# Kernel optimization log

Measured on AMD Instinct MI355X. Metric: run time of the kernel, lower is better.

Reference implementation:

```python
import jax, jax.numpy as jnp
from jax import lax
import numpy as np

B, M = 16384, 200            # flattened batch (B*TT), tokens per observation
NUM_LAYERS, GW, GH = 22, 11, 11
CNN_CH, HIDDEN = 128, 512
ACTION_NVEC = (9, 10)

MAX_VEC = jnp.array([9.0, 1.0, 1.0, 10.0, 3.0, 254.0, 1.0, 1.0, 235.0, 8.0, 9.0,
                     250.0, 29.0, 1.0, 1.0, 8.0, 1.0, 1.0, 6.0, 3.0, 1.0, 2.0],
                    jnp.float32)[None, :, None, None]  # [1,22,1,1]


def setup_inputs() -> dict:
    key = jax.random.key(0)
    ks = jax.random.split(key, 16)
    # compose coords byte so x,y nibbles are valid grid indices (0..10)
    xs = jax.random.randint(ks[0], (B, M), 0, GW)
    ys = jax.random.randint(ks[1], (B, M), 0, GH)
    coords = xs * 16 + ys
    atr = jax.random.randint(ks[2], (B, M), 0, NUM_LAYERS)
    val = jax.random.randint(ks[3], (B, M), 0, 11)
    observations = jnp.stack([coords, atr, val], axis=-1).astype(jnp.int32)  # [B,M,3]

    def nrm(k, shape, std=0.02):
        return (jax.random.normal(k, shape, jnp.float32) * std)

    return {
        "observations": observations,
        "conv1_w": nrm(ks[4], (CNN_CH, NUM_LAYERS, 5, 5)),
        "conv1_b": jnp.zeros((CNN_CH,), jnp.float32),
        "conv2_w": nrm(ks[5], (CNN_CH, CNN_CH, 3, 3)),
        "conv2_b": jnp.zeros((CNN_CH,), jnp.float32),
        "fc_w": nrm(ks[6], (HIDDEN // 2, CNN_CH)),
        "fc_b": jnp.zeros((HIDDEN // 2,), jnp.float32),
        "self_w": nrm(ks[7], (HIDDEN // 2, NUM_LAYERS)),
        "self_b": jnp.zeros((HIDDEN // 2,), jnp.float32),
        "actor0_w": nrm(ks[8], (ACTION_NVEC[0], HIDDEN), std=0.01),
        "actor0_b": jnp.zeros((ACTION_NVEC[0],), jnp.float32),
        "actor1_w": nrm(ks[9], (ACTION_NVEC[1], HIDDEN), std=0.01),
        "actor1_b": jnp.zeros((ACTION_NVEC[1],), jnp.float32),
        "value_w": nrm(ks[10], (1, HIDDEN)),
        "value_b": jnp.zeros((1,), jnp.float32),
    }


def reference(observations, conv1_w, conv1_b, conv2_w, conv2_b, fc_w, fc_b,
              self_w, self_b, actor0_w, actor0_b, actor1_w, actor1_b,
              value_w, value_b):
    obs = jnp.where(observations == 255, 0, observations)
    coords = obs[..., 0]
    xs = (coords >> 4) & 15
    ys = coords & 15
    atr = obs[..., 1]
    vals = obs[..., 2].astype(jnp.float32)           # [B,M]
    Bt = obs.shape[0]
    b_idx = jnp.broadcast_to(jnp.arange(Bt)[:, None], vals.shape)
    # masked scatter into dense grid (all tokens valid after 255->0 clamp)
    box = jnp.zeros((Bt, NUM_LAYERS, GW, GH), jnp.float32)
    box = box.at[b_idx, atr, xs, ys].set(vals, mode="drop")
    feats = box / MAX_VEC                            # [B,22,11,11]

    self_f = jax.nn.relu(feats[:, :, 5, 5] @ self_w.T + self_b)  # [B,256]

    dn = ("NCHW", "OIHW", "NCHW")
    h = lax.conv_general_dilated(feats, conv1_w, (3, 3), "VALID", dimension_numbers=dn)
    h = jax.nn.relu(h + conv1_b[None, :, None, None])            # [B,128,3,3]
    h = lax.conv_general_dilated(h, conv2_w, (1, 1), "VALID", dimension_numbers=dn)
    h = jax.nn.relu(h + conv2_b[None, :, None, None])            # [B,128,1,1]
    h = h.reshape(Bt, -1)
    cnn_f = jax.nn.relu(h @ fc_w.T + fc_b)                       # [B,256]

    hidden = jnp.concatenate([self_f, cnn_f], axis=1)            # [B,512]
    logits0 = hidden @ actor0_w.T + actor0_b
    logits1 = hidden @ actor1_w.T + actor1_b
    value = hidden @ value_w.T + value_b
    return (logits0, logits1, value)
```

## Files before the change

kernel.cpp:

```cpp
#include <hip/hip_runtime.h>

typedef unsigned short u16;
typedef __attribute__((ext_vector_type(8))) short short8;
typedef __attribute__((ext_vector_type(4))) float f32x4;

#define MFMA16(a, b, c) __builtin_amdgcn_mfma_f32_16x16x32_bf16((a), (b), (c), 0, 0, 0)

__device__ __forceinline__ u16 f2bf(float f) {
    unsigned u = __float_as_uint(f);
    unsigned r = (u + 0x7FFFu + ((u >> 16) & 1u)) >> 16;
    return (u16)r;
}

__device__ const float MAXV[22] = {9.f, 1.f, 1.f, 10.f, 3.f, 254.f, 1.f, 1.f, 235.f, 8.f, 9.f,
                                   250.f, 29.f, 1.f, 1.f, 8.f, 1.f, 1.f, 6.f, 3.f, 1.f, 2.f};

__global__ void prep_kernel(
    const float* c1w, const float* c1b, const float* c2w, const float* c2b,
    const float* fcw, const float* fcb, const float* sfw, const float* sfb,
    const float* a0w, const float* a0b, const float* a1w, const float* a1b,
    const float* vw, const float* vb,
    u16* W1F, u16* W2F, u16* FCF, u16* SELFF, u16* HEADF, float* BIAS)
{
    int idx = blockIdx.x * 256 + threadIdx.x;
    if (idx < 73728) {
        int grp = idx >> 9, off = idx & 511;
        int g = grp / 18, ks = grp - g * 18;
        int l = off >> 3, e = off & 7;
        int n = g * 16 + (l & 15);
        int k = ks * 32 + ((l >> 4) << 3) + e;
        float v = 0.f;
        if (k < 550) { int c = k / 25; v = c1w[n * 550 + k] * (1.0f / MAXV[c]); }
        W1F[idx] = f2bf(v);
    } else if (idx < 221184) {
        int j = idx - 73728;
        int grp = j >> 9, off = j & 511;
        int g = grp / 36, ks = grp - g * 36;
        int l = off >> 3, e = off & 7;
        int oc = g * 16 + (l & 15);
        int k = ks * 32 + ((l >> 4) << 3) + e;
        W2F[j] = f2bf(c2w[oc * 1152 + (k & 127) * 9 + (k >> 7)]);
    } else if (idx < 253952) {
        int j = idx - 221184;
        int grp = j >> 9, off = j & 511;
        int g = grp >> 2, kc = grp & 3;
        int l = off >> 3, e = off & 7;
        int n = g * 16 + (l & 15);
        int k = kc * 32 + ((l >> 4) << 3) + e;
        FCF[j] = f2bf(fcw[n * 128 + k]);
    } else if (idx < 262144) {
        int j = idx - 253952;
        int g = j >> 9, off = j & 511;
        int l = off >> 3, e = off & 7;
        int n = g * 16 + (l & 15);
        int k = ((l >> 4) << 3) + e;
        float v = (k < 22) ? sfw[n * 22 + k] * (1.0f / MAXV[k]) : 0.f;
        SELFF[j] = f2bf(v);
    } else if (idx < 278528) {
        int j = idx - 262144;
        int grp = j >> 9, off = j & 511;
        int g = grp >> 4, ks = grp & 15;
        int l = off >> 3, e = off & 7;
        int n = g * 16 + (l & 15);
        int k = ks * 32 + ((l >> 4) << 3) + e;
        float v = 0.f;
        if (n < 9) v = a0w[n * 512 + k];
        else if (n < 19) v = a1w[(n - 9) * 512 + k];
        else if (n == 19) v = vw[k];
        HEADF[j] = f2bf(v);
    } else if (idx < 279328) {
        int j = idx - 278528;
        float v = 0.f;
        if (j < 128) v = c1b[j];
        else if (j < 256) v = c2b[j - 128];
        else if (j < 512) v = fcb[j - 256];
        else if (j < 768) v = sfb[j - 512];
        else {
            int j2 = j - 768;
            if (j2 < 9) v = a0b[j2]; else if (j2 < 19) v = a1b[j2 - 9]; else if (j2 == 19) v = vb[0];
        }
        BIAS[j] = v;
    }
}

__global__ __launch_bounds__(256, 4) void k12_kernel(
    const int* __restrict__ obs, const u16* __restrict__ W1F,
    const float* __restrict__ BIAS, u16* __restrict__ h1F, u16* __restrict__ s22g)
{
    __shared__ __align__(16) u16 A[19968];
    const int tid = threadIdx.x, w = tid >> 6, l = tid & 63;
    const int s0 = blockIdx.x * 4;

    const int* myobs = obs + (long)(s0 + w) * 600;
    int tk[4][3];
    #pragma unroll
    for (int r = 0; r < 4; ++r) {
        int m = r * 64 + l; int mm = m < 200 ? m : 0;
        tk[r][0] = myobs[mm * 3]; tk[r][1] = myobs[mm * 3 + 1]; tk[r][2] = myobs[mm * 3 + 2];
    }

    {
        short8 z = {0, 0, 0, 0, 0, 0, 0, 0};
        int base = w * 621;
        int cnt = (w == 3) ? 633 : 621;
        for (int i = l; i < cnt; i += 64) *(short8*)(A + (base + i) * 8) = z;
    }
    __builtin_amdgcn_sched_barrier(0);

    #pragma unroll
    for (int r = 0; r < 4; ++r) {
        int m = r * 64 + l;
        int c = tk[r][0], a = tk[r][1], v = tk[r][2];
        c = (c == 255) ? 0 : c; a = (a == 255) ? 0 : a; v = (v == 255) ? 0 : v;
        int xs = (c >> 4) & 15, ys = c & 15;
        int ok = (m < 200) & ((unsigned)a < 22u) & (xs < 11) & (ys < 11);
        if (ok) {
            u16 bv = f2bf((float)v);
            int bcol = a * 25;
            #pragma unroll
            for (int ox = 0; ox < 3; ++ox) {
                int kx = xs - 3 * ox;
                if ((unsigned)kx > 4u) continue;
                #pragma unroll
                for (int oy = 0; oy < 3; ++oy) {
                    int ky = ys - 3 * oy;
                    if ((unsigned)ky > 4u) continue;
                    int row = w * 9 + ox * 3 + oy;
                    A[row * 552 + bcol + kx * 5 + ky] = bv;
                }
            }
        }
        __builtin_amdgcn_sched_barrier(0);
    }
    if (l < 32) {
        int row = w * 9 + 4;
        s22g[(s0 + w) * 32 + l] = A[row * 552 + l * 25 + 12];
    }
    __syncthreads();

    int Aoff[3];
    #pragma unroll
    for (int mt = 0; mt < 3; ++mt) {
        int row = mt * 16 + (l & 15);
        row = row < 36 ? row : 35;
        Aoff[mt] = (row * 552 + ((l >> 4) << 3)) << 1;
    }
    const u16* Wp0 = W1F + ((w * 2 + 0) * 18 << 9) + l * 8;
    const u16* Wp1 = W1F + ((w * 2 + 1) * 18 << 9) + l * 8;

    f32x4 acc[3][2];
    const f32x4 fz = {0.f, 0.f, 0.f, 0.f};
    #pragma unroll
    for (int i = 0; i < 3; ++i) { acc[i][0] = fz; acc[i][1] = fz; }

    short8 rb0[3], rb1[3];
    #pragma unroll
    for (int d = 0; d < 3; ++d) {
        rb0[d] = *(const short8*)(Wp0 + d * 512);
        rb1[d] = *(const short8*)(Wp1 + d * 512);
    }
    __builtin_amdgcn_s_setprio(1);
    #pragma unroll
    for (int ks = 0; ks < 18; ++ks) {
        const int sl = ks % 3;
        short8 b0 = rb0[sl], b1 = rb1[sl];
        if (ks < 15) {
            rb0[sl] = *(const short8*)(Wp0 + (ks + 3) * 512);
            rb1[sl] = *(const short8*)(Wp1 + (ks + 3) * 512);
        }
        short8 a0 = *(const short8*)((const char*)A + Aoff[0] + ks * 64);
        short8 a1 = *(const short8*)((const char*)A + Aoff[1] + ks * 64);
        short8 a2 = *(const short8*)((const char*)A + Aoff[2] + ks * 64);
        acc[0][0] = MFMA16(a0, b0, acc[0][0]);
        acc[0][1] = MFMA16(a0, b1, acc[0][1]);
        acc[1][0] = MFMA16(a1, b0, acc[1][0]);
        acc[1][1] = MFMA16(a1, b1, acc[1][1]);
        acc[2][0] = MFMA16(a2, b0, acc[2][0]);
        acc[2][1] = MFMA16(a2, b1, acc[2][1]);
    }
    __builtin_amdgcn_s_setprio(0);
    __syncthreads();

    u16* R = (u16*)A;
    #pragma unroll
    for (int mt = 0; mt < 3; ++mt) {
        #pragma unroll
        for (int nt = 0; nt < 2; ++nt) {
            int col = w * 32 + nt * 16 + (l & 15);
            float bias = BIAS[col];
            int hif = nt * 2 + ((l & 15) >> 3);
            int ef = l & 7;
            #pragma unroll
            for (int r = 0; r < 4; ++r) {
                int row = mt * 16 + ((l >> 4) << 2) + r;
                if (row < 36) {
                    int ds = row / 9;
                    int pos = row - ds * 9;
                    int ks = pos * 4 + w;
                    float v = acc[mt][nt][r] + bias;
                    v = v > 0.f ? v : 0.f;
                    R[(ks * 16 + hif * 4 + ds) * 8 + ef] = f2bf(v);
                }
            }
        }
    }
    __syncthreads();
    {
        const long Cbase = (long)(s0 >> 4) * 18432 + (s0 & 15) * 8;
        #pragma unroll
        for (int q = 0; q < 3; ++q) {
            int slot = tid + q * 256;
            if (slot < 576) {
                int ks = slot >> 4, lf = slot & 15;
                *(short8*)(h1F + Cbase + ks * 512 + (lf >> 2) * 128 + (lf & 3) * 8) =
                    *(const short8*)(R + slot * 8);
            }
        }
    }
}

__global__ __launch_bounds__(256, 2) void k3a_kernel(
    const u16* __restrict__ h1F, const u16* __restrict__ W2F,
    const float* __restrict__ BIAS, u16* __restrict__ a3F)
{
    const int tid = threadIdx.x, w = tid >> 6, l = tid & 63;
    const int sb = blockIdx.x * 2, s0 = blockIdx.x * 32;
    const float* c2b = BIAS + 128;
    const f32x4 fz = {0.f, 0.f, 0.f, 0.f};
    f32x4 acc[2][2];
    acc[0][0] = fz; acc[0][1] = fz; acc[1][0] = fz; acc[1][1] = fz;

    const u16* A0p = h1F + (long)(sb + 0) * 18432 + l * 8;
    const u16* A1p = h1F + (long)(sb + 1) * 18432 + l * 8;
    const u16* B0p = W2F + ((w * 2 + 0) * 36 << 9) + l * 8;
    const u16* B1p = W2F + ((w * 2 + 1) * 36 << 9) + l * 8;

    short8 ra0[3], ra1[3], rb0[3], rb1[3];
    #pragma unroll
    for (int d = 0; d < 3; ++d) {
        ra0[d] = *(const short8*)(A0p + d * 512);
        ra1[d] = *(const short8*)(A1p + d * 512);
        rb0[d] = *(const short8*)(B0p + d * 512);
        rb1[d] = *(const short8*)(B1p + d * 512);
    }
    __builtin_amdgcn_s_setprio(1);
    #pragma unroll
    for (int ks = 0; ks < 36; ++ks) {
        const int sl = ks % 3;
        short8 a0 = ra0[sl], a1 = ra1[sl], b0 = rb0[sl], b1 = rb1[sl];
        if (ks < 33) {
            ra0[sl] = *(const short8*)(A0p + (ks + 3) * 512);
            ra1[sl] = *(const short8*)(A1p + (ks + 3) * 512);
            rb0[sl] = *(const short8*)(B0p + (ks + 3) * 512);
            rb1[sl] = *(const short8*)(B1p + (ks + 3) * 512);
        }
        acc[0][0] = MFMA16(a0, b0, acc[0][0]);
        acc[0][1] = MFMA16(a0, b1, acc[0][1]);
        acc[1][0] = MFMA16(a1, b0, acc[1][0]);
        acc[1][1] = MFMA16(a1, b1, acc[1][1]);
    }
    __builtin_amdgcn_s_setprio(0);

    #pragma unroll
    for (int mt = 0; mt < 2; ++mt) {
        #pragma unroll
        for (int nt = 0; nt < 2; ++nt) {
            int col = w * 32 + nt * 16 + (l & 15);
            float bias = c2b[col];
            #pragma unroll
            for (int r = 0; r < 4; ++r) {
                int row = mt * 16 + ((l >> 4) << 2) + r;
                int s = s0 + row;
                float v = acc[mt][nt][r] + bias; v = v > 0.f ? v : 0.f;
                long ad = (long)(s >> 4) * 2048 + (col >> 5) * 512 +
                          (s & 15) * 8 + (((col >> 3) & 3) << 7) + (col & 7);
                a3F[ad] = f2bf(v);
            }
        }
    }
}

__global__ __launch_bounds__(256, 4) void k3b_kernel(
    const u16* __restrict__ a3F, const u16* __restrict__ s22g,
    const u16* __restrict__ FCF, const u16* __restrict__ SELFF,
    const u16* __restrict__ HEADF, const float* __restrict__ BIAS,
    float* __restrict__ out, int B)
{
    __shared__ __align__(16) u16 HID[16 * 520];
    const int tid = threadIdx.x, w = tid >> 6, l = tid & 63;
    const int s0 = blockIdx.x * 16;
    const float* fcb = BIAS + 256;
    const float* sfb = BIAS + 512;
    const float* hdb = BIAS + 768;
    const f32x4 fz = {0.f, 0.f, 0.f, 0.f};

    f32x4 acc8[4];
    #pragma unroll
    for (int j = 0; j < 4; ++j) acc8[j] = fz;
    #pragma unroll
    for (int kc = 0; kc < 4; ++kc) {
        short8 a = *(const short8*)(a3F + (long)blockIdx.x * 2048 + kc * 512 + l * 8);
        #pragma unroll
        for (int nt = 0; nt < 4; ++nt) {
            short8 bf = *(const short8*)(FCF + (((w * 4 + nt) * 4 + kc) << 9) + l * 8);
            acc8[nt] = MFMA16(a, bf, acc8[nt]);
        }
    }
    #pragma unroll
    for (int nt = 0; nt < 4; ++nt) {
        int col = w * 64 + nt * 16 + (l & 15);
        float bias = fcb[col];
        #pragma unroll
        for (int r = 0; r < 4; ++r) {
            int row = ((l >> 4) << 2) + r;
            float v = acc8[nt][r] + bias; v = v > 0.f ? v : 0.f;
            HID[row * 520 + 256 + col] = f2bf(v);
        }
    }

    {
        f32x4 acc9[4];
        #pragma unroll
        for (int j = 0; j < 4; ++j) acc9[j] = fz;
        short8 a = *(const short8*)(s22g + (s0 + (l & 15)) * 32 + ((l >> 4) << 3));
        #pragma unroll
        for (int nt = 0; nt < 4; ++nt) {
            short8 bs = *(const short8*)(SELFF + ((w * 4 + nt) << 9) + l * 8);
            acc9[nt] = MFMA16(a, bs, acc9[nt]);
        }
        #pragma unroll
        for (int nt = 0; nt < 4; ++nt) {
            int col = w * 64 + nt * 16 + (l & 15);
            float bias = sfb[col];
            #pragma unroll
            for (int r = 0; r < 4; ++r) {
                int row = ((l >> 4) << 2) + r;
                float v = acc9[nt][r] + bias; v = v > 0.f ? v : 0.f;
                HID[row * 520 + col] = f2bf(v);
            }
        }
    }
    __syncthreads();

    if (w < 2) {
        f32x4 hacc = fz;
        #pragma unroll
        for (int ks = 0; ks < 16; ++ks) {
            short8 a = *(const short8*)(HID + (l & 15) * 520 + ks * 32 + ((l >> 4) << 3));
            short8 b = *(const short8*)(HEADF + ((w * 16 + ks) << 9) + l * 8);
            hacc = MFMA16(a, b, hacc);
        }
        #pragma unroll
        for (int r = 0; r < 4; ++r) {
            int srow = s0 + ((l >> 4) << 2) + r;
            int col = w * 16 + (l & 15);
            float v = hacc[r] + hdb[col];
            if (col < 9) out[(long)srow * 9 + col] = v;
            else if (col < 19) out[(long)B * 9 + (long)srow * 10 + (col - 9)] = v;
            else if (col == 19) out[(long)B * 19 + srow] = v;
        }
    }
}

extern "C" void kernel_launch(void* const* d_in, const int* in_sizes, int n_in,
                              void* d_out, int out_size, void* d_ws, size_t ws_size,
                              hipStream_t stream)
{
    const int*   obs = (const int*)d_in[0];
    const float* c1w = (const float*)d_in[1];
    const float* c1b = (const float*)d_in[2];
    const float* c2w = (const float*)d_in[3];
    const float* c2b = (const float*)d_in[4];
    const float* fcw = (const float*)d_in[5];
    const float* fcb = (const float*)d_in[6];
    const float* sfw = (const float*)d_in[7];
    const float* sfb = (const float*)d_in[8];
    const float* a0w = (const float*)d_in[9];
    const float* a0b = (const float*)d_in[10];
    const float* a1w = (const float*)d_in[11];
    const float* a1b = (const float*)d_in[12];
    const float* vw  = (const float*)d_in[13];
    const float* vb  = (const float*)d_in[14];
    const int B = in_sizes[0] / 600;

    char* ws = (char*)d_ws;
    u16*   W1F   = (u16*)(ws + 0);
    u16*   W2F   = (u16*)(ws + 147456);
    u16*   FCF   = (u16*)(ws + 442368);
    u16*   SELFF = (u16*)(ws + 507904);
    u16*   HEADF = (u16*)(ws + 524288);
    float* BIAS  = (float*)(ws + 557056);
    u16*   s22g  = (u16*)(ws + 560256);
    u16*   h1F   = (u16*)(ws + 560256 + (size_t)B * 64);
    u16*   a3F   = (u16*)(ws + 560256 + (size_t)B * 64 + (size_t)B * 2304);

    prep_kernel<<<1092, 256, 0, stream>>>(c1w, c1b, c2w, c2b, fcw, fcb, sfw, sfb,
                                          a0w, a0b, a1w, a1b, vw, vb,
                                          W1F, W2F, FCF, SELFF, HEADF, BIAS);
    k12_kernel<<<B / 4, 256, 0, stream>>>(obs, W1F, BIAS, h1F, s22g);
    k3a_kernel<<<B / 32, 256, 0, stream>>>(h1F, W2F, BIAS, a3F);
    k3b_kernel<<<B / 16, 256, 0, stream>>>(a3F, s22g, FCF, SELFF, HEADF, BIAS,
                                           (float*)d_out, B);
}
```

Before: 68.77 us.

## Fuse conv2 and FC/head kernels into one kernel via shared memory

Merges the conv2 GEMM kernel with the fc/self/head kernel so the conv2 activations stay in LDS instead of going through global memory. The fused kernel works on 32 samples per block, using two M-tiles in the fc and self GEMMs, and all four waves now take part in the head GEMM. This removes one kernel launch and the a3F global write and read. In exchange it uses more LDS per block, about 41KB, which may limit occupancy at the requested two blocks per SM.

```diff
diff --git a/kernel.cpp b/kernel.cpp
--- a/kernel.cpp
+++ b/kernel.cpp
@@ -219,14 +219,22 @@
     }
 }
 
-__global__ __launch_bounds__(256, 2) void k3a_kernel(
-    const u16* __restrict__ h1F, const u16* __restrict__ W2F,
-    const float* __restrict__ BIAS, u16* __restrict__ a3F)
+__global__ __launch_bounds__(256, 2) void k3_kernel(
+    const u16* __restrict__ h1F, const u16* __restrict__ s22g,
+    const u16* __restrict__ W2F, const u16* __restrict__ FCF,
+    const u16* __restrict__ SELFF, const u16* __restrict__ HEADF,
+    const float* __restrict__ BIAS, float* __restrict__ out, int B)
 {
+    __shared__ __align__(16) u16 A3[32 * 136];
+    __shared__ __align__(16) u16 HID[32 * 520];
     const int tid = threadIdx.x, w = tid >> 6, l = tid & 63;
     const int sb = blockIdx.x * 2, s0 = blockIdx.x * 32;
     const float* c2b = BIAS + 128;
+    const float* fcb = BIAS + 256;
+    const float* sfb = BIAS + 512;
+    const float* hdb = BIAS + 768;
     const f32x4 fz = {0.f, 0.f, 0.f, 0.f};
+
     f32x4 acc[2][2];
     acc[0][0] = fz; acc[0][1] = fz; acc[1][0] = fz; acc[1][1] = fz;
 
@@ -270,90 +278,90 @@
             #pragma unroll
             for (int r = 0; r < 4; ++r) {
                 int row = mt * 16 + ((l >> 4) << 2) + r;
-                int s = s0 + row;
                 float v = acc[mt][nt][r] + bias; v = v > 0.f ? v : 0.f;
-                long ad = (long)(s >> 4) * 2048 + (col >> 5) * 512 +
-                          (s & 15) * 8 + (((col >> 3) & 3) << 7) + (col & 7);
-                a3F[ad] = f2bf(v);
-            }
-        }
-    }
-}
-
-__global__ __launch_bounds__(256, 4) void k3b_kernel(
-    const u16* __restrict__ a3F, const u16* __restrict__ s22g,
-    const u16* __restrict__ FCF, const u16* __restrict__ SELFF,
-    const u16* __restrict__ HEADF, const float* __restrict__ BIAS,
-    float* __restrict__ out, int B)
-{
-    __shared__ __align__(16) u16 HID[16 * 520];
-    const int tid = threadIdx.x, w = tid >> 6, l = tid & 63;
-    const int s0 = blockIdx.x * 16;
-    const float* fcb = BIAS + 256;
-    const float* sfb = BIAS + 512;
-    const float* hdb = BIAS + 768;
-    const f32x4 fz = {0.f, 0.f, 0.f, 0.f};
-
-    f32x4 acc8[4];
-    #pragma unroll
-    for (int j = 0; j < 4; ++j) acc8[j] = fz;
+                A3[row * 136 + col] = f2bf(v);
+            }
+        }
+    }
+    __syncthreads();
+
+    f32x4 acc8[2][4];
+    #pragma unroll
+    for (int i = 0; i < 2; ++i)
+        #pragma unroll
+        for (int j = 0; j < 4; ++j) acc8[i][j] = fz;
     #pragma unroll
     for (int kc = 0; kc < 4; ++kc) {
-        short8 a = *(const short8*)(a3F + (long)blockIdx.x * 2048 + kc * 512 + l * 8);
+        short8 a[2];
+        #pragma unroll
+        for (int mt = 0; mt < 2; ++mt)
+            a[mt] = *(const short8*)(A3 + (mt * 16 + (l & 15)) * 136 + kc * 32 + ((l >> 4) << 3));
         #pragma unroll
         for (int nt = 0; nt < 4; ++nt) {
             short8 bf = *(const short8*)(FCF + (((w * 4 + nt) * 4 + kc) << 9) + l * 8);
-            acc8[nt] = MFMA16(a, bf, acc8[nt]);
-        }
-    }
-    #pragma unroll
-    for (int nt = 0; nt < 4; ++nt) {
-        int col = w * 64 + nt * 16 + (l & 15);
-        float bias = fcb[col];
-        #pragma unroll
-        for (int r = 0; r < 4; ++r) {
-            int row = ((l >> 4) << 2) + r;
-            float v = acc8[nt][r] + bias; v = v > 0.f ? v : 0.f;
-            HID[row * 520 + 256 + col] = f2bf(v);
-        }
-    }
+            acc8[0][nt] = MFMA16(a[0], bf, acc8[0][nt]);
+            acc8[1][nt] = MFMA16(a[1], bf, acc8[1][nt]);
+        }
+    }
+    #pragma unroll
+    for (int mt = 0; mt < 2; ++mt)
+        #pragma unroll
+        for (int nt = 0; nt < 4; ++nt) {
+            int col = w * 64 + nt * 16 + (l & 15);
+            float bias = fcb[col];
+            #pragma unroll
+            for (int r = 0; r < 4; ++r) {
+                int row = mt * 16 + ((l >> 4) << 2) + r;
+                float v = acc8[mt][nt][r] + bias; v = v > 0.f ? v : 0.f;
+                HID[row * 520 + 256 + col] = f2bf(v);
+            }
+        }
 
     {
-        f32x4 acc9[4];
-        #pragma unroll
-        for (int j = 0; j < 4; ++j) acc9[j] = fz;
-        short8 a = *(const short8*)(s22g + (s0 + (l & 15)) * 32 + ((l >> 4) << 3));
+        f32x4 acc9[2][4];
+        #pragma unroll
+        for (int i = 0; i < 2; ++i)
+            #pragma unroll
+            for (int j = 0; j < 4; ++j) acc9[i][j] = fz;
+        short8 a[2];
+        #pragma unroll
+        for (int mt = 0; mt < 2; ++mt)
+            a[mt] = *(const short8*)(s22g + (s0 + mt * 16 + (l & 15)) * 32 + ((l >> 4) << 3));
         #pragma unroll
         for (int nt = 0; nt < 4; ++nt) {
             short8 bs = *(const short8*)(SELFF + ((w * 4 + nt) << 9) + l * 8);
-            acc9[nt] = MFMA16(a, bs, acc9[nt]);
-        }
-        #pragma unroll
-        for (int nt = 0; nt < 4; ++nt) {
-            int col = w * 64 + nt * 16 + (l & 15);
-            float bias = sfb[col];
-            #pragma unroll
-            for (int r = 0; r < 4; ++r) {
-                int row = ((l >> 4) << 2) + r;
-                float v = acc9[nt][r] + bias; v = v > 0.f ? v : 0.f;
-                HID[row * 520 + col] = f2bf(v);
-            }
-        }
+            acc9[0][nt] = MFMA16(a[0], bs, acc9[0][nt]);
+            acc9[1][nt] = MFMA16(a[1], bs, acc9[1][nt]);
+        }
+        #pragma unroll
+        for (int mt = 0; mt < 2; ++mt)
+            #pragma unroll
+            for (int nt = 0; nt < 4; ++nt) {
+                int col = w * 64 + nt * 16 + (l & 15);
+                float bias = sfb[col];
+                #pragma unroll
+                for (int r = 0; r < 4; ++r) {
+                    int row = mt * 16 + ((l >> 4) << 2) + r;
+                    float v = acc9[mt][nt][r] + bias; v = v > 0.f ? v : 0.f;
+                    HID[row * 520 + col] = f2bf(v);
+                }
+            }
     }
     __syncthreads();
 
-    if (w < 2) {
+    {
         f32x4 hacc = fz;
+        const int mt = w & 1, ct = w >> 1;
         #pragma unroll
         for (int ks = 0; ks < 16; ++ks) {
-            short8 a = *(const short8*)(HID + (l & 15) * 520 + ks * 32 + ((l >> 4) << 3));
-            short8 b = *(const short8*)(HEADF + ((w * 16 + ks) << 9) + l * 8);
+            short8 a = *(const short8*)(HID + (mt * 16 + (l & 15)) * 520 + ks * 32 + ((l >> 4) << 3));
+            short8 b = *(const short8*)(HEADF + ((ct * 16 + ks) << 9) + l * 8);
             hacc = MFMA16(a, b, hacc);
         }
         #pragma unroll
         for (int r = 0; r < 4; ++r) {
-            int srow = s0 + ((l >> 4) << 2) + r;
-            int col = w * 16 + (l & 15);
+            int srow = s0 + mt * 16 + ((l >> 4) << 2) + r;
+            int col = ct * 16 + (l & 15);
             float v = hacc[r] + hdb[col];
             if (col < 9) out[(long)srow * 9 + col] = v;
             else if (col < 19) out[(long)B * 9 + (long)srow * 10 + (col - 9)] = v;
@@ -392,13 +400,11 @@
     float* BIAS  = (float*)(ws + 557056);
     u16*   s22g  = (u16*)(ws + 560256);
     u16*   h1F   = (u16*)(ws + 560256 + (size_t)B * 64);
-    u16*   a3F   = (u16*)(ws + 560256 + (size_t)B * 64 + (size_t)B * 2304);
 
     prep_kernel<<<1092, 256, 0, stream>>>(c1w, c1b, c2w, c2b, fcw, fcb, sfw, sfb,
                                           a0w, a0b, a1w, a1b, vw, vb,
                                           W1F, W2F, FCF, SELFF, HEADF, BIAS);
     k12_kernel<<<B / 4, 256, 0, stream>>>(obs, W1F, BIAS, h1F, s22g);
-    k3a_kernel<<<B / 32, 256, 0, stream>>>(h1F, W2F, BIAS, a3F);
-    k3b_kernel<<<B / 16, 256, 0, stream>>>(a3F, s22g, FCF, SELFF, HEADF, BIAS,
-                                           (float*)d_out, B);
+    k3_kernel<<<B / 32, 256, 0, stream>>>(h1F, s22g, W2F, FCF, SELFF, HEADF, BIAS,
+                                          (float*)d_out, B);
 }
```

Measured after the change: 64.12 us (median of 2 runs). -6.8%, faster.
